# Optimization experiments

Measured on AMD Instinct MI355X. Metric: run time of the kernel, lower is better.

## Reference

```python
import jax, jax.numpy as jnp
import numpy as np
from jax import lax

B, C, H, W = 4, 64, 256, 256
T, Q = 16, 0.2
C2 = 2 * C


def conv2d(x, w, b, pad):
    y = lax.conv_general_dilated(x, w, (1, 1), [(pad, pad), (pad, pad)],
                                 dimension_numbers=('NCHW', 'OIHW', 'NCHW'))
    return y + b[None, :, None, None]


def setup_inputs() -> dict:
    key = jax.random.key(0)
    ks = jax.random.split(key, 10)
    x = jax.random.normal(ks[0], (B, C, H, W), dtype=jnp.float32)
    lms = jax.random.normal(ks[1], (B, 4, H, W), dtype=jnp.float32)
    # params (kaiming-ish scale)
    W_conv = jax.random.normal(ks[2], (C2, C, 3, 3), dtype=jnp.float32) * (1.0 / np.sqrt(C * 9))
    b_conv = jnp.zeros((C2,), dtype=jnp.float32)
    W_out = jax.random.normal(ks[3], (4, C2), dtype=jnp.float32) * (1.0 / np.sqrt(C2))  # 1x1 conv as matrix
    b_out = jnp.zeros((4,), dtype=jnp.float32)
    W_aue = jax.random.normal(ks[4], (4, C2, 3, 3), dtype=jnp.float32) * (1.0 / np.sqrt(C2 * 9))
    b_aue = jnp.zeros((4,), dtype=jnp.float32)
    # T Bernoulli(1-q) channel masks, fixed for reproducibility  [T, 2C]
    masks = jax.random.bernoulli(ks[5], 1.0 - Q, (T, C2)).astype(jnp.float32)
    return {"x": x, "lms": lms, "W_conv": W_conv, "b_conv": b_conv,
            "W_out": W_out, "b_out": b_out, "W_aue": W_aue, "b_aue": b_aue,
            "masks": masks}


def reference(x, lms, W_conv, b_conv, W_out, b_out, W_aue, b_aue, masks):
    # feature extraction: 3x3 conv C -> 2C
    h = conv2d(x, W_conv, b_conv, 1)                      # [B, 2C, H, W]
    # MC-dropout samples: out(mask_t * h) == (W_out * mask_t) @ h  (1x1 conv is linear)
    Wt = W_out[None, :, :] * masks[:, None, :]            # [T, 4, 2C]
    samples = jnp.tanh(jnp.einsum('toc,bchw->tbohw', Wt, h)
                       + b_out[None, None, :, None, None]) + lms[None]  # [T, B, 4, H, W]
    mean = jnp.mean(samples, axis=0)
    EU = jnp.var(samples, axis=0, ddof=1)                 # unbiased variance over T
    AU = jax.nn.sigmoid(conv2d(h, W_aue, b_aue, 1))       # [B, 4, H, W]
    return (AU, EU, mean)
```

## Files before the change

kernel.cpp:

```cpp
#include <hip/hip_runtime.h>

#define Bsz 4
#define Cin 64
#define C2c 128
#define Hh 256
#define Ww 256
#define Tt 16
#define HW (Hh*Ww)
#define PLANE (Bsz*4*HW)

typedef __attribute__((ext_vector_type(8))) short bf16x8;
typedef __attribute__((ext_vector_type(4))) float f32x4;

#define XT_OFF  0
#define WBF_OFF 33554432
#define WTB_OFF 33701888
#define AUB_OFF 33718272
#define ZP_OFF  33727488

#define N_WTB 8192
#define N_WBF 73728
#define N_AUB 4608
#define N_ZP  64

__device__ __forceinline__ unsigned short f2bf(float f) {
  union { float f; unsigned u; } cv; cv.f = f;
  unsigned u = cv.u;
  unsigned r = (u + 0x7fffu + ((u >> 16) & 1u)) >> 16;
  return (unsigned short)r;
}

__device__ __forceinline__ unsigned cvtpk(float a, float b) {
  unsigned r;
  asm("v_cvt_pk_bf16_f32 %0, %1, %2" : "=v"(r) : "v"(a), "v"(b));
  return r;
}

union U8 { uint2 u2[2]; uint4 u4; bf16x8 v; };

#define GLOAD16(g, l) __builtin_amdgcn_global_load_lds( \
    (const __attribute__((address_space(1))) unsigned int*)(g), \
    (__attribute__((address_space(3))) unsigned int*)(l), 16, 0, 0)

__global__ __launch_bounds__(256) void xt2_kernel(
    const float* __restrict__ x, const float* __restrict__ W_out,
    const float* __restrict__ masks, const float* __restrict__ Wc,
    const float* __restrict__ W_aue,
    unsigned short* __restrict__ xT, unsigned short* __restrict__ Wtb,
    unsigned short* __restrict__ Wbf, unsigned short* __restrict__ Aub,
    unsigned short* __restrict__ Zp) {
  const int tid = threadIdx.x;

  if (blockIdx.x >= 1024) {
    int i = (blockIdx.x - 1024) * 256 + tid;
    if (i < N_WTB) {
      int to = i >> 7, c = i & 127;
      int t = to >> 2, o = to & 3;
      Wtb[i] = f2bf(W_out[o * C2c + c] * masks[t * C2c + c]);
    } else if (i < N_WTB + N_WBF) {
      int idx = i - N_WTB;
      int j = idx & 7;
      int lane = (idx >> 3) & 63;
      int nt = (idx >> 9) & 7;
      int c = idx >> 12;
      int qq = lane >> 4;
      int tap = c >> 1;
      int ic = (c & 1) * 32 + qq * 8 + j;
      int n = nt * 16 + (lane & 15);
      Wbf[idx] = f2bf(Wc[((size_t)n * Cin + ic) * 9 + tap]);
    } else if (i < N_WTB + N_WBF + N_AUB) {
      int idx = i - N_WTB - N_WBF;
      int m = idx / 1152, k = idx % 1152;
      int tap = k >> 7, c = k & 127;
      Aub[idx] = f2bf(W_aue[((size_t)m * C2c + c) * 9 + tap]);
    } else if (i < N_WTB + N_WBF + N_AUB + N_ZP) {
      Zp[i - N_WTB - N_WBF - N_AUB] = 0;
    }
    return;
  }

  int gid = blockIdx.x * 256 + tid;
  int px = gid & 65535, bi = gid >> 16;
  const float* xp = x + ((size_t)bi << 22) + px;
  unsigned short* op = xT + ((size_t)gid << 6);
  #pragma unroll
  for (int gp = 0; gp < 4; ++gp) {
    float v[16];
    #pragma unroll
    for (int k = 0; k < 16; ++k) v[k] = xp[((size_t)(gp * 16 + k)) << 16];
    uint4 a, b;
    a.x = cvtpk(v[0], v[1]);   a.y = cvtpk(v[2], v[3]);
    a.z = cvtpk(v[4], v[5]);   a.w = cvtpk(v[6], v[7]);
    b.x = cvtpk(v[8], v[9]);   b.y = cvtpk(v[10], v[11]);
    b.z = cvtpk(v[12], v[13]); b.w = cvtpk(v[14], v[15]);
    *(uint4*)(op + gp * 16) = a;
    *(uint4*)(op + gp * 16 + 8) = b;
  }
}

__global__ __launch_bounds__(256, 3) void fused_kernel(
    const unsigned short* __restrict__ xT, const unsigned short* __restrict__ Wbf,
    const unsigned short* __restrict__ Wtb, const unsigned short* __restrict__ Aub,
    const unsigned short* __restrict__ Zp,
    const float* __restrict__ bc, const float* __restrict__ b_out,
    const float* __restrict__ b_aue, const float* __restrict__ lms,
    float* __restrict__ out) {
  __shared__ __align__(16) unsigned short sh[23040];
  const int tid = threadIdx.x;
  const int x0 = blockIdx.x * 16, y0 = blockIdx.y * 8, bi = blockIdx.z;

  #pragma unroll
  for (int hf = 0; hf < 2; ++hf) {
    #pragma unroll
    for (int i = 0; i < 4; ++i) {
      int g = i * 256 + tid;
      int r = g >> 2;
      int l = (g & 3) ^ ((r >> 1) & 3);
      int pr = r / 20, pc = r - pr * 20;
      int gy = y0 - 2 + pr, gx = x0 - 2 + pc;
      bool ok = (r < 240) && ((unsigned)gy < Hh) && ((unsigned)gx < Ww);
      const unsigned short* src = ok
        ? xT + (((size_t)bi * Hh + gy) * Ww + gx) * Cin + (hf * 4 + l) * 8
        : Zp;
      GLOAD16(src, &sh[hf * 8192 + g * 8]);
    }
  }

  const int lane = tid & 63, wv = tid >> 6;
  const int n16 = lane & 15, q = lane >> 4;
  const int ph = wv >> 1, oh = wv & 1;

  int rbase[6];
  #pragma unroll
  for (int s = 0; s < 6; ++s) {
    int px = ph * 96 + s * 16 + n16;
    int pr = px / 18, pc = px % 18;
    rbase[s] = pr * 20 + pc;
  }

  f32x4 acc[6][4];
  #pragma unroll
  for (int s = 0; s < 6; ++s)
    #pragma unroll
    for (int mt = 0; mt < 4; ++mt) acc[s][mt] = (f32x4){0.f, 0.f, 0.f, 0.f};

  asm volatile("s_waitcnt vmcnt(4)" ::: "memory");
  __builtin_amdgcn_s_barrier();
  __builtin_amdgcn_sched_barrier(0);

  #pragma unroll
  for (int hf = 0; hf < 2; ++hf) {
    if (hf == 1) {
      asm volatile("s_waitcnt vmcnt(0)" ::: "memory");
      __builtin_amdgcn_s_barrier();
      __builtin_amdgcn_sched_barrier(0);
    }
    #pragma unroll
    for (int tap = 0; tap < 9; ++tap) {
      const int dd = (tap / 3) * 20 + (tap % 3);
      const int c = tap * 2 + hf;
      bf16x8 wfr[4];
      const unsigned short* wb = Wbf + ((size_t)(c * 8 + oh * 4) * 64 + lane) * 8;
      #pragma unroll
      for (int mt = 0; mt < 4; ++mt)
        wfr[mt] = ((const U8*)(wb + mt * 512))->v;
      __builtin_amdgcn_s_setprio(1);
      #pragma unroll
      for (int s = 0; s < 6; ++s) {
        int rr = rbase[s] + dd;
        int a = hf * 8192 + rr * 32 + ((q ^ ((rr >> 1) & 3)) << 3);
        U8 t; t.u4 = *(const uint4*)(&sh[a]);
        #pragma unroll
        for (int mt = 0; mt < 4; ++mt)
          acc[s][mt] =
            __builtin_amdgcn_mfma_f32_16x16x32_bf16(wfr[mt], t.v, acc[s][mt], 0, 0, 0);
      }
      __builtin_amdgcn_s_setprio(0);
    }
  }
  __syncthreads();

  #pragma unroll
  for (int s = 0; s < 6; ++s) {
    const int px = ph * 96 + s * 16 + n16;
    if (px < 180) {
      const int pr = px / 18, pc = px % 18;
      const int gy = y0 - 1 + pr, gx = x0 - 1 + pc;
      const bool valid = ((unsigned)gy < Hh) && ((unsigned)gx < Ww);
      const int key = px & 15;
      #pragma unroll
      for (int mt = 0; mt < 4; ++mt) {
        const int oc0 = oh * 64 + mt * 16 + q * 4;
        const float4 b4 = *(const float4*)(bc + oc0);
        unsigned lo = cvtpk(acc[s][mt][0] + b4.x, acc[s][mt][1] + b4.y);
        unsigned hi = cvtpk(acc[s][mt][2] + b4.z, acc[s][mt][3] + b4.w);
        if (!valid) { lo = 0u; hi = 0u; }
        int a = px * 128 + (((oc0 >> 3) ^ key) << 3) + (q & 1) * 4;
        *(uint2*)(&sh[a]) = make_uint2(lo, hi);
      }
    }
  }
  __syncthreads();

  f32x4 accG[2][4];
  f32x4 accA[2];
  #pragma unroll
  for (int nt = 0; nt < 2; ++nt) {
    accA[nt] = (f32x4){0.f, 0.f, 0.f, 0.f};
    #pragma unroll
    for (int mt = 0; mt < 4; ++mt) accG[nt][mt] = (f32x4){0.f, 0.f, 0.f, 0.f};
  }

  #pragma unroll
  for (int kc = 0; kc < 4; ++kc) {
    bf16x8 afr[4];
    #pragma unroll
    for (int mt = 0; mt < 4; ++mt)
      afr[mt] = ((const U8*)(Wtb + (size_t)(mt * 16 + n16) * C2c + kc * 32 + q * 8))->v;
    #pragma unroll
    for (int nt = 0; nt < 2; ++nt) {
      int hr = (wv * 2 + nt + 1) * 18 + n16 + 1;
      int a = hr * 128 + (((kc * 4 + q) ^ (hr & 15)) << 3);
      U8 b; b.u4 = *(const uint4*)(&sh[a]);
      #pragma unroll
      for (int mt = 0; mt < 4; ++mt)
        accG[nt][mt] = __builtin_amdgcn_mfma_f32_16x16x32_bf16(afr[mt], b.v, accG[nt][mt], 0, 0, 0);
    }
  }

  #pragma unroll
  for (int kc = 0; kc < 36; ++kc) {
    const int tap = kc >> 2, co4 = kc & 3;
    const int dy = tap / 3, dx = tap % 3;
    bf16x8 afr = ((const U8*)(Aub + (size_t)(n16 & 3) * 1152 + kc * 32 + q * 8))->v;
    #pragma unroll
    for (int nt = 0; nt < 2; ++nt) {
      int hr = (wv * 2 + nt + dy) * 18 + n16 + dx;
      int a = hr * 128 + (((co4 * 4 + q) ^ (hr & 15)) << 3);
      U8 b; b.u4 = *(const uint4*)(&sh[a]);
      accA[nt] = __builtin_amdgcn_mfma_f32_16x16x32_bf16(afr, b.v, accA[nt], 0, 0, 0);
    }
  }

  const float b0 = b_out[0], b1 = b_out[1], b2 = b_out[2], b3 = b_out[3];
  const float ba = b_aue[q];
  const int px = x0 + n16;
  #pragma unroll
  for (int nt = 0; nt < 2; ++nt) {
    const int y = y0 + wv * 2 + nt;
    float th[4][4];
    #pragma unroll
    for (int mt = 0; mt < 4; ++mt) {
      #pragma unroll
      for (int r = 0; r < 4; ++r) {
        float bo = (r == 0) ? b0 : (r == 1) ? b1 : (r == 2) ? b2 : b3;
        float v = accG[nt][mt][r] + bo;
        float e = __expf(2.f * v);
        th[mt][r] = 1.f - 2.f / (e + 1.f);
      }
    }
    float mean_r[4], eu_r[4];
    #pragma unroll
    for (int r = 0; r < 4; ++r) {
      float s = th[0][r] + th[1][r] + th[2][r] + th[3][r];
      s += __shfl_xor(s, 16);
      s += __shfl_xor(s, 32);
      float m = s * (1.f / 16.f);
      float d0 = th[0][r] - m, d1 = th[1][r] - m, d2 = th[2][r] - m, d3 = th[3][r] - m;
      float vs = d0 * d0 + d1 * d1 + d2 * d2 + d3 * d3;
      vs += __shfl_xor(vs, 16);
      vs += __shfl_xor(vs, 32);
      mean_r[r] = m;
      eu_r[r] = vs * (1.f / 15.f);
    }
    float au_r[4];
    #pragma unroll
    for (int r = 0; r < 4; ++r) au_r[r] = __shfl(accA[nt][r], n16);

    float m_q  = (q == 0) ? mean_r[0] : (q == 1) ? mean_r[1] : (q == 2) ? mean_r[2] : mean_r[3];
    float eu_q = (q == 0) ? eu_r[0]   : (q == 1) ? eu_r[1]   : (q == 2) ? eu_r[2]   : eu_r[3];
    float au_q = (q == 0) ? au_r[0]   : (q == 1) ? au_r[1]   : (q == 2) ? au_r[2]   : au_r[3];
    au_q = 1.f / (1.f + __expf(-(au_q + ba)));
    size_t oidx = ((size_t)(bi * 4 + q)) * HW + (size_t)y * Ww + px;
    float lm = lms[oidx];
    out[oidx] = au_q;
    out[PLANE + oidx] = eu_q;
    out[2 * (size_t)PLANE + oidx] = m_q + lm;
  }
}

extern "C" void kernel_launch(void* const* d_in, const int* in_sizes, int n_in,
                              void* d_out, int out_size, void* d_ws, size_t ws_size,
                              hipStream_t stream) {
  const float* x      = (const float*)d_in[0];
  const float* lms    = (const float*)d_in[1];
  const float* W_conv = (const float*)d_in[2];
  const float* b_conv = (const float*)d_in[3];
  const float* W_out  = (const float*)d_in[4];
  const float* b_out  = (const float*)d_in[5];
  const float* W_aue  = (const float*)d_in[6];
  const float* b_aue  = (const float*)d_in[7];
  const float* masks  = (const float*)d_in[8];
  float* out = (float*)d_out;

  char* ws = (char*)d_ws;
  unsigned short* xT  = (unsigned short*)(ws + XT_OFF);
  unsigned short* Wbf = (unsigned short*)(ws + WBF_OFF);
  unsigned short* Wtb = (unsigned short*)(ws + WTB_OFF);
  unsigned short* Aub = (unsigned short*)(ws + AUB_OFF);
  unsigned short* Zp  = (unsigned short*)(ws + ZP_OFF);

  xt2_kernel<<<dim3(1363), dim3(256), 0, stream>>>(x, W_out, masks, W_conv, W_aue,
                                                   xT, Wtb, Wbf, Aub, Zp);
  fused_kernel<<<dim3(16, 32, 4), dim3(256), 0, stream>>>(xT, Wbf, Wtb, Aub, Zp, b_conv,
                                                          b_out, b_aue, lms, out);
}
```

Baseline: 217.4 us.

## Stage conv features in two channel halves and transpose input via LDS

The fused kernel now writes the 128-channel conv output to shared memory one 64-channel half at a time. It accumulates the 1x1 head and the AU 3x3 conv over each half in turn, which shrinks LDS from about 45KB to 32KB and raises the launch-bounds occupancy target from 3 to 5 blocks. The NCHW to NHWC bf16 conversion kernel now does coalesced float4 row loads and transposes through LDS, replacing strided per-pixel gathers. The cost is an extra barrier round and two serialized write phases, and register pressure at the higher occupancy target could cause spills.

```diff
diff --git a/kernel.cpp b/kernel.cpp
--- a/kernel.cpp
+++ b/kernel.cpp
@@ -42,17 +42,18 @@
     (const __attribute__((address_space(1))) unsigned int*)(g), \
     (__attribute__((address_space(3))) unsigned int*)(l), 16, 0, 0)
 
-__global__ __launch_bounds__(256) void xt2_kernel(
+__global__ __launch_bounds__(256) void xtp_kernel(
     const float* __restrict__ x, const float* __restrict__ W_out,
     const float* __restrict__ masks, const float* __restrict__ Wc,
     const float* __restrict__ W_aue,
     unsigned short* __restrict__ xT, unsigned short* __restrict__ Wtb,
     unsigned short* __restrict__ Wbf, unsigned short* __restrict__ Aub,
     unsigned short* __restrict__ Zp) {
+  __shared__ unsigned short xs[64 * 132];
   const int tid = threadIdx.x;
 
-  if (blockIdx.x >= 1024) {
-    int i = (blockIdx.x - 1024) * 256 + tid;
+  if (blockIdx.z == 4) {
+    int i = (blockIdx.y * 2 + blockIdx.x) * 256 + tid;
     if (i < N_WTB) {
       int to = i >> 7, c = i & 127;
       int t = to >> 2, o = to & 3;
@@ -79,33 +80,34 @@
     return;
   }
 
-  int gid = blockIdx.x * 256 + tid;
-  int px = gid & 65535, bi = gid >> 16;
-  const float* xp = x + ((size_t)bi << 22) + px;
-  unsigned short* op = xT + ((size_t)gid << 6);
-  #pragma unroll
-  for (int gp = 0; gp < 4; ++gp) {
-    float v[16];
-    #pragma unroll
-    for (int k = 0; k < 16; ++k) v[k] = xp[((size_t)(gp * 16 + k)) << 16];
-    uint4 a, b;
-    a.x = cvtpk(v[0], v[1]);   a.y = cvtpk(v[2], v[3]);
-    a.z = cvtpk(v[4], v[5]);   a.w = cvtpk(v[6], v[7]);
-    b.x = cvtpk(v[8], v[9]);   b.y = cvtpk(v[10], v[11]);
-    b.z = cvtpk(v[12], v[13]); b.w = cvtpk(v[14], v[15]);
-    *(uint4*)(op + gp * 16) = a;
-    *(uint4*)(op + gp * 16 + 8) = b;
-  }
-}
-
-__global__ __launch_bounds__(256, 3) void fused_kernel(
+  const int x0 = blockIdx.x * 128, y = blockIdx.y, bi = blockIdx.z;
+  #pragma unroll
+  for (int i = 0; i < 8; ++i) {
+    int idx = i * 256 + tid;
+    int ic = idx >> 5, xq = idx & 31;
+    float4 v = *(const float4*)(x + (((size_t)bi * Cin + ic) * Hh + y) * Ww + x0 + xq * 4);
+    *(uint2*)(&xs[ic * 132 + xq * 4]) = make_uint2(cvtpk(v.x, v.y), cvtpk(v.z, v.w));
+  }
+  __syncthreads();
+  #pragma unroll
+  for (int j = 0; j < 4; ++j) {
+    int idx = j * 256 + tid;
+    int px = idx >> 3, icg = idx & 7;
+    unsigned short u[8];
+    #pragma unroll
+    for (int k = 0; k < 8; ++k) u[k] = xs[(icg * 8 + k) * 132 + px];
+    *(uint4*)(xT + (((size_t)bi * Hh + y) * Ww + (x0 + px)) * Cin + icg * 8) = *(uint4*)u;
+  }
+}
+
+__global__ __launch_bounds__(256, 5) void fused_kernel(
     const unsigned short* __restrict__ xT, const unsigned short* __restrict__ Wbf,
     const unsigned short* __restrict__ Wtb, const unsigned short* __restrict__ Aub,
     const unsigned short* __restrict__ Zp,
     const float* __restrict__ bc, const float* __restrict__ b_out,
     const float* __restrict__ b_aue, const float* __restrict__ lms,
     float* __restrict__ out) {
-  __shared__ __align__(16) unsigned short sh[23040];
+  __shared__ __align__(16) unsigned short sh[16384];
   const int tid = threadIdx.x;
   const int x0 = blockIdx.x * 16, y0 = blockIdx.y * 8, bi = blockIdx.z;
 
@@ -180,28 +182,6 @@
   }
   __syncthreads();
 
-  #pragma unroll
-  for (int s = 0; s < 6; ++s) {
-    const int px = ph * 96 + s * 16 + n16;
-    if (px < 180) {
-      const int pr = px / 18, pc = px % 18;
-      const int gy = y0 - 1 + pr, gx = x0 - 1 + pc;
-      const bool valid = ((unsigned)gy < Hh) && ((unsigned)gx < Ww);
-      const int key = px & 15;
-      #pragma unroll
-      for (int mt = 0; mt < 4; ++mt) {
-        const int oc0 = oh * 64 + mt * 16 + q * 4;
-        const float4 b4 = *(const float4*)(bc + oc0);
-        unsigned lo = cvtpk(acc[s][mt][0] + b4.x, acc[s][mt][1] + b4.y);
-        unsigned hi = cvtpk(acc[s][mt][2] + b4.z, acc[s][mt][3] + b4.w);
-        if (!valid) { lo = 0u; hi = 0u; }
-        int a = px * 128 + (((oc0 >> 3) ^ key) << 3) + (q & 1) * 4;
-        *(uint2*)(&sh[a]) = make_uint2(lo, hi);
-      }
-    }
-  }
-  __syncthreads();
-
   f32x4 accG[2][4];
   f32x4 accA[2];
   #pragma unroll
@@ -212,34 +192,66 @@
   }
 
   #pragma unroll
-  for (int kc = 0; kc < 4; ++kc) {
-    bf16x8 afr[4];
-    #pragma unroll
-    for (int mt = 0; mt < 4; ++mt)
-      afr[mt] = ((const U8*)(Wtb + (size_t)(mt * 16 + n16) * C2c + kc * 32 + q * 8))->v;
-    #pragma unroll
-    for (int nt = 0; nt < 2; ++nt) {
-      int hr = (wv * 2 + nt + 1) * 18 + n16 + 1;
-      int a = hr * 128 + (((kc * 4 + q) ^ (hr & 15)) << 3);
-      U8 b; b.u4 = *(const uint4*)(&sh[a]);
+  for (int half = 0; half < 2; ++half) {
+    if (oh == half) {
+      #pragma unroll
+      for (int s = 0; s < 6; ++s) {
+        const int px = ph * 96 + s * 16 + n16;
+        if (px < 180) {
+          const int pr = px / 18, pc = px % 18;
+          const int gy = y0 - 1 + pr, gx = x0 - 1 + pc;
+          const bool valid = ((unsigned)gy < Hh) && ((unsigned)gx < Ww);
+          const int key = px & 7;
+          #pragma unroll
+          for (int mt = 0; mt < 4; ++mt) {
+            const int ocl = mt * 16 + q * 4;
+            const float4 b4 = *(const float4*)(bc + half * 64 + ocl);
+            unsigned lo = cvtpk(acc[s][mt][0] + b4.x, acc[s][mt][1] + b4.y);
+            unsigned hi = cvtpk(acc[s][mt][2] + b4.z, acc[s][mt][3] + b4.w);
+            if (!valid) { lo = 0u; hi = 0u; }
+            int a = px * 64 + ((((ocl >> 3)) ^ key) << 3) + (q & 1) * 4;
+            *(uint2*)(&sh[a]) = make_uint2(lo, hi);
+          }
+        }
+      }
+    }
+    __syncthreads();
+
+    #pragma unroll
+    for (int kk = 0; kk < 2; ++kk) {
+      const int kc = half * 2 + kk;
+      bf16x8 afr[4];
       #pragma unroll
       for (int mt = 0; mt < 4; ++mt)
-        accG[nt][mt] = __builtin_amdgcn_mfma_f32_16x16x32_bf16(afr[mt], b.v, accG[nt][mt], 0, 0, 0);
-    }
-  }
-
-  #pragma unroll
-  for (int kc = 0; kc < 36; ++kc) {
-    const int tap = kc >> 2, co4 = kc & 3;
-    const int dy = tap / 3, dx = tap % 3;
-    bf16x8 afr = ((const U8*)(Aub + (size_t)(n16 & 3) * 1152 + kc * 32 + q * 8))->v;
-    #pragma unroll
-    for (int nt = 0; nt < 2; ++nt) {
-      int hr = (wv * 2 + nt + dy) * 18 + n16 + dx;
-      int a = hr * 128 + (((co4 * 4 + q) ^ (hr & 15)) << 3);
-      U8 b; b.u4 = *(const uint4*)(&sh[a]);
-      accA[nt] = __builtin_amdgcn_mfma_f32_16x16x32_bf16(afr, b.v, accA[nt], 0, 0, 0);
-    }
+        afr[mt] = ((const U8*)(Wtb + (size_t)(mt * 16 + n16) * C2c + kc * 32 + q * 8))->v;
+      #pragma unroll
+      for (int nt = 0; nt < 2; ++nt) {
+        int hr = (wv * 2 + nt + 1) * 18 + n16 + 1;
+        int a = hr * 64 + (((kk * 4 + q) ^ (hr & 7)) << 3);
+        U8 b; b.u4 = *(const uint4*)(&sh[a]);
+        #pragma unroll
+        for (int mt = 0; mt < 4; ++mt)
+          accG[nt][mt] = __builtin_amdgcn_mfma_f32_16x16x32_bf16(afr[mt], b.v, accG[nt][mt], 0, 0, 0);
+      }
+    }
+
+    #pragma unroll
+    for (int t9 = 0; t9 < 9; ++t9) {
+      const int dy = t9 / 3, dx = t9 % 3;
+      #pragma unroll
+      for (int cc = 0; cc < 2; ++cc) {
+        const int kc = t9 * 4 + half * 2 + cc;
+        bf16x8 afr = ((const U8*)(Aub + (size_t)(n16 & 3) * 1152 + kc * 32 + q * 8))->v;
+        #pragma unroll
+        for (int nt = 0; nt < 2; ++nt) {
+          int hr = (wv * 2 + nt + dy) * 18 + n16 + dx;
+          int a = hr * 64 + (((cc * 4 + q) ^ (hr & 7)) << 3);
+          U8 b; b.u4 = *(const uint4*)(&sh[a]);
+          accA[nt] = __builtin_amdgcn_mfma_f32_16x16x32_bf16(afr, b.v, accA[nt], 0, 0, 0);
+        }
+      }
+    }
+    if (half == 0) __syncthreads();
   }
 
   const float b0 = b_out[0], b1 = b_out[1], b2 = b_out[2], b3 = b_out[3];
@@ -310,8 +322,8 @@
   unsigned short* Aub = (unsigned short*)(ws + AUB_OFF);
   unsigned short* Zp  = (unsigned short*)(ws + ZP_OFF);
 
-  xt2_kernel<<<dim3(1363), dim3(256), 0, stream>>>(x, W_out, masks, W_conv, W_aue,
-                                                   xT, Wtb, Wbf, Aub, Zp);
+  xtp_kernel<<<dim3(2, 256, 5), dim3(256), 0, stream>>>(x, W_out, masks, W_conv, W_aue,
+                                                        xT, Wtb, Wbf, Aub, Zp);
   fused_kernel<<<dim3(16, 32, 4), dim3(256), 0, stream>>>(xT, Wbf, Wtb, Aub, Zp, b_conv,
                                                           b_out, b_aue, lms, out);
 }
```

Result: slower. 849.8 us (+290.9%).
